# Kernel optimization log

Hardware: AMD Instinct MI355X
Metric: run time of the kernel (lower is better)

## Reference

```python
import jax, jax.numpy as jnp
import numpy as np

H = W = 28  # fixed grid size hardcoded in the module
ATOL = 1e-8  # torch.allclose(v, 0.0) default tolerance


def setup_inputs() -> dict:
    key = jax.random.key(0)
    k1, k2, k3 = jax.random.split(key, 3)
    B = 32768
    x = jax.random.normal(k1, (B, 1, H, W), dtype=jnp.float32)
    # pos2d: integer grid (as in reset_parameters) plus small learned jitter
    g0, g1 = jnp.meshgrid(jnp.arange(H, dtype=jnp.float32),
                          jnp.arange(W, dtype=jnp.float32), indexing='ij')
    grid = jnp.stack([g0, g1], axis=-1)  # [28,28,2]
    pos2d = grid + 0.5 * jax.random.normal(k2, (H, W, 2), dtype=jnp.float32)
    # weight: around the 0.167 init value
    weight = 0.167 + 0.05 * jax.random.uniform(k3, (H, W), dtype=jnp.float32)
    return {"input": x, "pos2d": pos2d, "weight": weight}


def reference(input, pos2d, weight):
    # input: [B,1,28,28]; pos2d: [28,28,2]; weight: [28,28]
    x = input[:, 0]                       # [B,28,28]
    sw = jax.nn.relu(weight)              # [28,28]
    ce = jnp.round(pos2d)                 # rounded centers, [28,28,2]
    acc = jnp.zeros_like(x)
    # fixed 5x5 deformable neighborhood (25 structurally distinct offsets)
    for i0 in range(-2, 3):
        for i1 in range(-2, 3):
            off = jnp.array([i0, i1], dtype=pos2d.dtype)
            cr = ce + off                 # neighbor coords (float, integer-valued)
            cri = cr.astype(jnp.int32)
            in_b = ((cri[..., 0] >= 0) & (cri[..., 0] < H) &
                    (cri[..., 1] >= 0) & (cri[..., 1] < W))  # [28,28]
            idx0 = jnp.clip(cri[..., 0], 0, H - 1)
            idx1 = jnp.clip(cri[..., 1], 0, W - 1)
            v = x[:, idx0, idx1]          # [B,28,28] gather (same idx per batch)
            v = jnp.where(in_b[None], v, 0.0)
            # torch.allclose(v, 0.0) short-circuit: tiny values treated as 0
            v = jnp.where(jnp.abs(v) <= ATOL, 0.0, v)
            dis = cr - pos2d              # distance to learned center
            w = jnp.exp(-0.5 * jnp.sum(dis * dis, axis=-1))  # [28,28]
            acc = acc + v * w[None]
    out = acc * sw[None]
    return out[:, None]                   # [B,1,28,28]
```

## Files before the change

### kernel.cpp

```cpp
#include <hip/hip_runtime.h>

#define HH 28
#define WW 28
#define NPIX 784
#define BLOCK 832

__global__ __launch_bounds__(BLOCK, 1) void axs_89807766159734_kernel(
    const float* __restrict__ x, const float* __restrict__ pos2d,
    const float* __restrict__ weight, float* __restrict__ out,
    int nGroups)
{
    __shared__ float4 lds[NPIX];
    const int p = threadIdx.x;
    const bool act = p < NPIX;

    float coef[25];
    int   boff[25];
    if (act) {
        const float p0 = pos2d[2*p],   p1 = pos2d[2*p + 1];
        const float sw = fmaxf(weight[p], 0.0f);
        const float ce0 = rintf(p0), ce1 = rintf(p1);
#pragma unroll
        for (int t = 0; t < 25; ++t) {
            const int i0 = t / 5 - 2, i1 = t % 5 - 2;
            const float cr0 = ce0 + (float)i0, cr1 = ce1 + (float)i1;
            const int c0 = (int)cr0, c1 = (int)cr1;
            const bool inb = (c0 >= 0) & (c0 < HH) & (c1 >= 0) & (c1 < WW);
            const int q0 = min(max(c0, 0), HH - 1);
            const int q1 = min(max(c1, 0), WW - 1);
            const float d0 = cr0 - p0, d1 = cr1 - p1;
            const float w = __expf(-0.5f * (d0*d0 + d1*d1));
            coef[t] = inb ? sw * w : 0.0f;
            boff[t] = (q0 * WW + q1) * 16;
        }
    }

    int g = blockIdx.x;
    float v0 = 0.f, v1 = 0.f, v2 = 0.f, v3 = 0.f;
    if (g < nGroups && act) {
        const size_t base = (size_t)g * 4u * NPIX;
        v0 = x[base + p];
        v1 = x[base + NPIX + p];
        v2 = x[base + 2*NPIX + p];
        v3 = x[base + 3*NPIX + p];
    }

    for (; g < nGroups; g += gridDim.x) {
        __syncthreads();
        if (act) lds[p] = make_float4(v0, v1, v2, v3);
        __syncthreads();

        const int gn = g + gridDim.x;
        if (gn < nGroups && act) {
            const size_t nb = (size_t)gn * 4u * NPIX;
            v0 = x[nb + p];
            v1 = x[nb + NPIX + p];
            v2 = x[nb + 2*NPIX + p];
            v3 = x[nb + 3*NPIX + p];
        }

        if (act) {
            float a0 = 0.f, a1 = 0.f, a2 = 0.f, a3 = 0.f;
#pragma unroll
            for (int t = 0; t < 25; ++t) {
                const float4 v = *(const float4*)((const char*)lds + boff[t]);
                const float c = coef[t];
                a0 = fmaf(c, v.x, a0);
                a1 = fmaf(c, v.y, a1);
                a2 = fmaf(c, v.z, a2);
                a3 = fmaf(c, v.w, a3);
            }
            const size_t base = (size_t)g * 4u * NPIX;
            out[base + p]          = a0;
            out[base + NPIX + p]   = a1;
            out[base + 2*NPIX + p] = a2;
            out[base + 3*NPIX + p] = a3;
        }
    }
}

extern "C" void kernel_launch(void* const* d_in, const int* in_sizes, int n_in,
                              void* d_out, int out_size, void* d_ws, size_t ws_size,
                              hipStream_t stream) {
    const float* x      = (const float*)d_in[0];
    const float* pos2d  = (const float*)d_in[1];
    const float* weight = (const float*)d_in[2];
    float* out = (float*)d_out;

    const int B = in_sizes[0] / NPIX;
    const int nGroups = B / 4;
    int blocks = nGroups < 1024 ? nGroups : 1024;

    hipLaunchKernelGGL(axs_89807766159734_kernel, dim3(blocks), dim3(BLOCK), 0, stream,
                       x, pos2d, weight, out, nGroups);
}
```

Measured before the change: 195.2 us.

## Pad LDS image, reorder pixels by bank, double-buffer results for coalesced stores

Stores each 4-image group in a zero-padded 36x40 LDS tile, so the 5x5 neighbourhood uses fixed offsets and no bounds clamping. Threads are remapped to pixels by sorting them on the LDS bank of their window base, which is meant to cut bank conflicts on the gathers. Results go into double-buffered LDS and are written back coalesced one iteration later. The gaussian weights are factored into separable row and column terms. The launch bound occupancy hint also changes. In exchange the kernel uses much more LDS, adds setup syncs and atomics, and makes the global writes depend on an extra LDS round trip.

```diff
diff --git a/kernel.cpp b/kernel.cpp
--- a/kernel.cpp
+++ b/kernel.cpp
@@ -4,78 +4,146 @@
 #define WW 28
 #define NPIX 784
 #define BLOCK 832
+#define PSTRIDE 40
+#define PROWS 36
+#define PSLOTS (PROWS * PSTRIDE)
 
-__global__ __launch_bounds__(BLOCK, 1) void axs_89807766159734_kernel(
+__global__ __launch_bounds__(BLOCK, 7) void axs_89807766159734_kernel(
     const float* __restrict__ x, const float* __restrict__ pos2d,
     const float* __restrict__ weight, float* __restrict__ out,
     int nGroups)
 {
-    __shared__ float4 lds[NPIX];
-    const int p = threadIdx.x;
-    const bool act = p < NPIX;
+    __shared__ float4 img[PSLOTS];
+    __shared__ float4 resA[NPIX];
+    __shared__ float4 resB[NPIX];
+    __shared__ unsigned short ordered[NPIX];
+    __shared__ unsigned short ovf[NPIX];
+    __shared__ int cnt[16];
+    __shared__ int ovfn;
 
-    float coef[25];
-    int   boff[25];
+    const int tid = threadIdx.x;
+    const bool act = tid < NPIX;
+
+    for (int s = tid; s < PSLOTS; s += BLOCK) img[s] = make_float4(0.f, 0.f, 0.f, 0.f);
+    if (act) ordered[tid] = 0xFFFFu;
+    if (tid < 16) cnt[tid] = 0;
+    if (tid == 0) ovfn = 0;
+    __syncthreads();
+
+    int K16 = 0, rank = 0;
     if (act) {
-        const float p0 = pos2d[2*p],   p1 = pos2d[2*p + 1];
-        const float sw = fmaxf(weight[p], 0.0f);
-        const float ce0 = rintf(p0), ce1 = rintf(p1);
+        const float p0 = pos2d[2 * tid], p1 = pos2d[2 * tid + 1];
+        const int c0 = (int)rintf(p0), c1 = (int)rintf(p1);
+        const int a0 = min(max(c0, -2), HH + 1);
+        const int a1 = min(max(c1, -2), WW + 1);
+        K16 = ((a0 + 2) * PSTRIDE + (a1 + 2)) & 15;
+        rank = atomicAdd(&cnt[K16], 1);
+    }
+    __syncthreads();
+    if (act) {
+        const int L = rank * 16 + K16;
+        if (L < NPIX) ordered[L] = (unsigned short)tid;
+        else          ovf[atomicAdd(&ovfn, 1)] = (unsigned short)tid;
+    }
+    __syncthreads();
+    if (act && ordered[tid] == 0xFFFFu) {
+        const int o = atomicAdd(&ovfn, -1) - 1;
+        ordered[tid] = ovf[o];
+    }
+    __syncthreads();
+
+    int ap = tid;
+    int base = 0;
+    float coef[5][5];
+    if (act) {
+        ap = ordered[tid];
+        const float p0 = pos2d[2 * ap], p1 = pos2d[2 * ap + 1];
+        const float sw = fmaxf(weight[ap], 0.f);
+        const float r0f = rintf(p0), r1f = rintf(p1);
+        const int c0 = (int)r0f, c1 = (int)r1f;
+        const float f0 = r0f - p0, f1 = r1f - p1;
+        float e0[5], e1[5];
 #pragma unroll
-        for (int t = 0; t < 25; ++t) {
-            const int i0 = t / 5 - 2, i1 = t % 5 - 2;
-            const float cr0 = ce0 + (float)i0, cr1 = ce1 + (float)i1;
-            const int c0 = (int)cr0, c1 = (int)cr1;
-            const bool inb = (c0 >= 0) & (c0 < HH) & (c1 >= 0) & (c1 < WW);
-            const int q0 = min(max(c0, 0), HH - 1);
-            const int q1 = min(max(c1, 0), WW - 1);
-            const float d0 = cr0 - p0, d1 = cr1 - p1;
-            const float w = __expf(-0.5f * (d0*d0 + d1*d1));
-            coef[t] = inb ? sw * w : 0.0f;
-            boff[t] = (q0 * WW + q1) * 16;
+        for (int k = 0; k < 5; ++k) {
+            const float d0 = f0 + (float)(k - 2);
+            const float d1 = f1 + (float)(k - 2);
+            const int rr = c0 + (k - 2), cc = c1 + (k - 2);
+            e0[k] = (rr >= 0 && rr < HH) ? sw * __expf(-0.5f * d0 * d0) : 0.f;
+            e1[k] = (cc >= 0 && cc < WW) ? __expf(-0.5f * d1 * d1) : 0.f;
         }
+#pragma unroll
+        for (int a = 0; a < 5; ++a)
+#pragma unroll
+            for (int b = 0; b < 5; ++b) coef[a][b] = e0[a] * e1[b];
+        const int a0 = min(max(c0, -2), HH + 1);
+        const int a1 = min(max(c1, -2), WW + 1);
+        base = ((a0 + 2) * PSTRIDE + (a1 + 2)) * 16;
     }
+    const int myslot = (tid / WW + 4) * PSTRIDE + (tid % WW) + 4;
 
     int g = blockIdx.x;
     float v0 = 0.f, v1 = 0.f, v2 = 0.f, v3 = 0.f;
-    if (g < nGroups && act) {
-        const size_t base = (size_t)g * 4u * NPIX;
-        v0 = x[base + p];
-        v1 = x[base + NPIX + p];
-        v2 = x[base + 2*NPIX + p];
-        v3 = x[base + 3*NPIX + p];
+    if (act && g < nGroups) {
+        const size_t b = (size_t)g * 4u * NPIX;
+        v0 = x[b + tid];
+        v1 = x[b + NPIX + tid];
+        v2 = x[b + 2 * NPIX + tid];
+        v3 = x[b + 3 * NPIX + tid];
     }
+
+    float4* rw = resA;
+    float4* rr = resB;
+    bool have_prev = false;
+    size_t prev_b = 0;
 
     for (; g < nGroups; g += gridDim.x) {
         __syncthreads();
-        if (act) lds[p] = make_float4(v0, v1, v2, v3);
+        if (act) img[myslot] = make_float4(v0, v1, v2, v3);
         __syncthreads();
 
         const int gn = g + gridDim.x;
-        if (gn < nGroups && act) {
+        if (act && gn < nGroups) {
             const size_t nb = (size_t)gn * 4u * NPIX;
-            v0 = x[nb + p];
-            v1 = x[nb + NPIX + p];
-            v2 = x[nb + 2*NPIX + p];
-            v3 = x[nb + 3*NPIX + p];
+            v0 = x[nb + tid];
+            v1 = x[nb + NPIX + tid];
+            v2 = x[nb + 2 * NPIX + tid];
+            v3 = x[nb + 3 * NPIX + tid];
         }
+        if (act && have_prev) {
+            const float4 r = rr[tid];
+            out[prev_b + tid]            = r.x;
+            out[prev_b + NPIX + tid]     = r.y;
+            out[prev_b + 2 * NPIX + tid] = r.z;
+            out[prev_b + 3 * NPIX + tid] = r.w;
+        }
+        if (act) {
+            float s0 = 0.f, s1 = 0.f, s2 = 0.f, s3 = 0.f;
+            const char* bp = (const char*)img + base;
+#pragma unroll
+            for (int i = 0; i < 5; ++i)
+#pragma unroll
+                for (int j = 0; j < 5; ++j) {
+                    const float4 v = *(const float4*)(bp + (i * PSTRIDE + j) * 16);
+                    const float c = coef[i][j];
+                    s0 = fmaf(c, v.x, s0);
+                    s1 = fmaf(c, v.y, s1);
+                    s2 = fmaf(c, v.z, s2);
+                    s3 = fmaf(c, v.w, s3);
+                }
+            rw[ap] = make_float4(s0, s1, s2, s3);
+        }
+        prev_b = (size_t)g * 4u * NPIX;
+        have_prev = true;
+        float4* t = rw; rw = rr; rr = t;
+    }
 
-        if (act) {
-            float a0 = 0.f, a1 = 0.f, a2 = 0.f, a3 = 0.f;
-#pragma unroll
-            for (int t = 0; t < 25; ++t) {
-                const float4 v = *(const float4*)((const char*)lds + boff[t]);
-                const float c = coef[t];
-                a0 = fmaf(c, v.x, a0);
-                a1 = fmaf(c, v.y, a1);
-                a2 = fmaf(c, v.z, a2);
-                a3 = fmaf(c, v.w, a3);
-            }
-            const size_t base = (size_t)g * 4u * NPIX;
-            out[base + p]          = a0;
-            out[base + NPIX + p]   = a1;
-            out[base + 2*NPIX + p] = a2;
-            out[base + 3*NPIX + p] = a3;
-        }
+    __syncthreads();
+    if (act && have_prev) {
+        const float4 r = rr[tid];
+        out[prev_b + tid]            = r.x;
+        out[prev_b + NPIX + tid]     = r.y;
+        out[prev_b + 2 * NPIX + tid] = r.z;
+        out[prev_b + 3 * NPIX + tid] = r.w;
     }
 }
 
```

Result: slower. 201.5 us (+3.2%).

## Use zero-padded LDS image with single base offset and separable Gaussian weights

Applied to the files above, without the earlier changes.

Stores each 4-image group in a zero-padded 36x40 LDS tile, so every thread addresses its 25 taps from one base pointer with compile-time immediate offsets instead of 25 per-tap offset registers. The Gaussian weights are computed as products of per-axis exponentials (10 exps instead of 25), and out-of-range taps get zero weight and read the zero padding. The launch-bounds hint changes from 1 to 7, which may let the compiler trade registers for occupancy, but the padded LDS tile (about 23 KB) could limit how many blocks fit per CU. The tiny-value zeroing from the reference (|v| <= 1e-8) is not applied here, as it was not before either.

```diff
diff --git a/kernel.cpp b/kernel.cpp
--- a/kernel.cpp
+++ b/kernel.cpp
@@ -4,77 +4,103 @@
 #define WW 28
 #define NPIX 784
 #define BLOCK 832
+#define PSTRIDE 40
+#define PROWS 36
+#define PSLOTS (PROWS * PSTRIDE)
 
-__global__ __launch_bounds__(BLOCK, 1) void axs_89807766159734_kernel(
+__global__ __launch_bounds__(BLOCK, 7) void axs_89807766159734_kernel(
     const float* __restrict__ x, const float* __restrict__ pos2d,
     const float* __restrict__ weight, float* __restrict__ out,
     int nGroups)
 {
-    __shared__ float4 lds[NPIX];
-    const int p = threadIdx.x;
-    const bool act = p < NPIX;
+    __shared__ float4 img[PSLOTS];
+    const int tid = threadIdx.x;
+    const bool act = tid < NPIX;
 
-    float coef[25];
-    int   boff[25];
+    for (int s = tid; s < PSLOTS; s += BLOCK)
+        img[s] = make_float4(0.f, 0.f, 0.f, 0.f);
+
+    float c00=0,c01=0,c02=0,c03=0,c04=0,
+          c10=0,c11=0,c12=0,c13=0,c14=0,
+          c20=0,c21=0,c22=0,c23=0,c24=0,
+          c30=0,c31=0,c32=0,c33=0,c34=0,
+          c40=0,c41=0,c42=0,c43=0,c44=0;
+    int base = 0;
     if (act) {
-        const float p0 = pos2d[2*p],   p1 = pos2d[2*p + 1];
-        const float sw = fmaxf(weight[p], 0.0f);
-        const float ce0 = rintf(p0), ce1 = rintf(p1);
-#pragma unroll
-        for (int t = 0; t < 25; ++t) {
-            const int i0 = t / 5 - 2, i1 = t % 5 - 2;
-            const float cr0 = ce0 + (float)i0, cr1 = ce1 + (float)i1;
-            const int c0 = (int)cr0, c1 = (int)cr1;
-            const bool inb = (c0 >= 0) & (c0 < HH) & (c1 >= 0) & (c1 < WW);
-            const int q0 = min(max(c0, 0), HH - 1);
-            const int q1 = min(max(c1, 0), WW - 1);
-            const float d0 = cr0 - p0, d1 = cr1 - p1;
-            const float w = __expf(-0.5f * (d0*d0 + d1*d1));
-            coef[t] = inb ? sw * w : 0.0f;
-            boff[t] = (q0 * WW + q1) * 16;
-        }
+        const float p0 = pos2d[2 * tid], p1 = pos2d[2 * tid + 1];
+        const float sw = fmaxf(weight[tid], 0.0f);
+        const float r0 = rintf(p0), r1 = rintf(p1);
+        const int i0 = (int)r0, i1 = (int)r1;
+        const float f0 = r0 - p0, f1 = r1 - p1;
+
+        const float d0m2 = f0 - 2.f, d0m1 = f0 - 1.f, d0p1 = f0 + 1.f, d0p2 = f0 + 2.f;
+        const float e0m2 = (i0 - 2 >= 0 && i0 - 2 < HH) ? sw * __expf(-0.5f * d0m2 * d0m2) : 0.f;
+        const float e0m1 = (i0 - 1 >= 0 && i0 - 1 < HH) ? sw * __expf(-0.5f * d0m1 * d0m1) : 0.f;
+        const float e0z  = (i0     >= 0 && i0     < HH) ? sw * __expf(-0.5f * f0   * f0  ) : 0.f;
+        const float e0p1 = (i0 + 1 >= 0 && i0 + 1 < HH) ? sw * __expf(-0.5f * d0p1 * d0p1) : 0.f;
+        const float e0p2 = (i0 + 2 >= 0 && i0 + 2 < HH) ? sw * __expf(-0.5f * d0p2 * d0p2) : 0.f;
+
+        const float d1m2 = f1 - 2.f, d1m1 = f1 - 1.f, d1p1 = f1 + 1.f, d1p2 = f1 + 2.f;
+        const float e1m2 = (i1 - 2 >= 0 && i1 - 2 < WW) ? __expf(-0.5f * d1m2 * d1m2) : 0.f;
+        const float e1m1 = (i1 - 1 >= 0 && i1 - 1 < WW) ? __expf(-0.5f * d1m1 * d1m1) : 0.f;
+        const float e1z  = (i1     >= 0 && i1     < WW) ? __expf(-0.5f * f1   * f1  ) : 0.f;
+        const float e1p1 = (i1 + 1 >= 0 && i1 + 1 < WW) ? __expf(-0.5f * d1p1 * d1p1) : 0.f;
+        const float e1p2 = (i1 + 2 >= 0 && i1 + 2 < WW) ? __expf(-0.5f * d1p2 * d1p2) : 0.f;
+
+        c00 = e0m2*e1m2; c01 = e0m2*e1m1; c02 = e0m2*e1z; c03 = e0m2*e1p1; c04 = e0m2*e1p2;
+        c10 = e0m1*e1m2; c11 = e0m1*e1m1; c12 = e0m1*e1z; c13 = e0m1*e1p1; c14 = e0m1*e1p2;
+        c20 = e0z *e1m2; c21 = e0z *e1m1; c22 = e0z *e1z; c23 = e0z *e1p1; c24 = e0z *e1p2;
+        c30 = e0p1*e1m2; c31 = e0p1*e1m1; c32 = e0p1*e1z; c33 = e0p1*e1p1; c34 = e0p1*e1p2;
+        c40 = e0p2*e1m2; c41 = e0p2*e1m1; c42 = e0p2*e1z; c43 = e0p2*e1p1; c44 = e0p2*e1p2;
+
+        const int a0c = min(max(i0, -2), HH + 1);
+        const int a1c = min(max(i1, -2), WW + 1);
+        base = ((a0c + 2) * PSTRIDE + (a1c + 2)) * 16;
     }
+    const int myslot = (tid / WW + 4) * PSTRIDE + (tid % WW) + 4;
 
     int g = blockIdx.x;
     float v0 = 0.f, v1 = 0.f, v2 = 0.f, v3 = 0.f;
-    if (g < nGroups && act) {
-        const size_t base = (size_t)g * 4u * NPIX;
-        v0 = x[base + p];
-        v1 = x[base + NPIX + p];
-        v2 = x[base + 2*NPIX + p];
-        v3 = x[base + 3*NPIX + p];
+    if (act && g < nGroups) {
+        const size_t b = (size_t)g * 4u * NPIX;
+        v0 = x[b + tid];
+        v1 = x[b + NPIX + tid];
+        v2 = x[b + 2 * NPIX + tid];
+        v3 = x[b + 3 * NPIX + tid];
     }
 
     for (; g < nGroups; g += gridDim.x) {
         __syncthreads();
-        if (act) lds[p] = make_float4(v0, v1, v2, v3);
+        if (act) img[myslot] = make_float4(v0, v1, v2, v3);
         __syncthreads();
 
         const int gn = g + gridDim.x;
-        if (gn < nGroups && act) {
+        if (act && gn < nGroups) {
             const size_t nb = (size_t)gn * 4u * NPIX;
-            v0 = x[nb + p];
-            v1 = x[nb + NPIX + p];
-            v2 = x[nb + 2*NPIX + p];
-            v3 = x[nb + 3*NPIX + p];
+            v0 = x[nb + tid];
+            v1 = x[nb + NPIX + tid];
+            v2 = x[nb + 2 * NPIX + tid];
+            v3 = x[nb + 3 * NPIX + tid];
         }
 
         if (act) {
             float a0 = 0.f, a1 = 0.f, a2 = 0.f, a3 = 0.f;
-#pragma unroll
-            for (int t = 0; t < 25; ++t) {
-                const float4 v = *(const float4*)((const char*)lds + boff[t]);
-                const float c = coef[t];
-                a0 = fmaf(c, v.x, a0);
-                a1 = fmaf(c, v.y, a1);
-                a2 = fmaf(c, v.z, a2);
-                a3 = fmaf(c, v.w, a3);
-            }
-            const size_t base = (size_t)g * 4u * NPIX;
-            out[base + p]          = a0;
-            out[base + NPIX + p]   = a1;
-            out[base + 2*NPIX + p] = a2;
-            out[base + 3*NPIX + p] = a3;
+            const char* bp = (const char*)img + base;
+#define TAP(I, J, C) do {                                                  \
+            const float4 tv = *(const float4*)(bp + ((I) * PSTRIDE + (J)) * 16); \
+            a0 = fmaf(C, tv.x, a0); a1 = fmaf(C, tv.y, a1);                \
+            a2 = fmaf(C, tv.z, a2); a3 = fmaf(C, tv.w, a3); } while (0)
+            TAP(0,0,c00); TAP(0,1,c01); TAP(0,2,c02); TAP(0,3,c03); TAP(0,4,c04);
+            TAP(1,0,c10); TAP(1,1,c11); TAP(1,2,c12); TAP(1,3,c13); TAP(1,4,c14);
+            TAP(2,0,c20); TAP(2,1,c21); TAP(2,2,c22); TAP(2,3,c23); TAP(2,4,c24);
+            TAP(3,0,c30); TAP(3,1,c31); TAP(3,2,c32); TAP(3,3,c33); TAP(3,4,c34);
+            TAP(4,0,c40); TAP(4,1,c41); TAP(4,2,c42); TAP(4,3,c43); TAP(4,4,c44);
+#undef TAP
+            const size_t b = (size_t)g * 4u * NPIX;
+            out[b + tid]            = a0;
+            out[b + NPIX + tid]     = a1;
+            out[b + 2 * NPIX + tid] = a2;
+            out[b + 3 * NPIX + tid] = a3;
         }
     }
 }
```

Measured after the change: 195.3 us. No clear change (+0.1%).
